# Kernel tuning notes

Hardware: AMD Instinct MI355X
Metric: run time of the kernel (lower is better)

The kernel has to match this reference:

```python
import jax, jax.numpy as jnp
import numpy as np

B, T, C = 32, 512, 32
D, H, DFF, NL = 512, 8, 2048, 3
P, STRIDE, PAD = 16, 8, 8
N = (T - P) // STRIDE + 2  # 64 patches
E = D // H


def _sinusoidal_pe(n, d):
    pos = np.arange(n, dtype=np.float32)[:, None]
    div = np.exp(np.arange(0, d, 2, dtype=np.float32) * -(np.log(10000.0) / d))
    pe = np.zeros((n, d), np.float32)
    pe[:, 0::2] = np.sin(pos * div)
    pe[:, 1::2] = np.cos(pos * div)
    return jnp.asarray(pe)


def setup_inputs() -> dict:
    key = jax.random.key(0)
    ks = jax.random.split(key, 16)
    s = 0.02
    inp = {
        'x_enc': jax.random.normal(ks[0], (B, T, C), jnp.float32),
        'W_val': jax.random.normal(ks[1], (P, D), jnp.float32) * s,
        'Wq': jax.random.normal(ks[2], (NL, D, D), jnp.float32) * s,
        'bq': jnp.zeros((NL, D), jnp.float32),
        'Wk': jax.random.normal(ks[3], (NL, D, D), jnp.float32) * s,
        'bk': jnp.zeros((NL, D), jnp.float32),
        'Wv': jax.random.normal(ks[4], (NL, D, D), jnp.float32) * s,
        'bv': jnp.zeros((NL, D), jnp.float32),
        'Wo': jax.random.normal(ks[5], (NL, D, D), jnp.float32) * s,
        'bo': jnp.zeros((NL, D), jnp.float32),
        'Wc1': jax.random.normal(ks[6], (NL, D, DFF), jnp.float32) * s,
        'bc1': jnp.zeros((NL, DFF), jnp.float32),
        'Wc2': jax.random.normal(ks[7], (NL, DFF, D), jnp.float32) * s,
        'bc2': jnp.zeros((NL, D), jnp.float32),
        'ln1_g': jnp.ones((NL, D), jnp.float32),
        'ln1_b': jnp.zeros((NL, D), jnp.float32),
        'ln2_g': jnp.ones((NL, D), jnp.float32),
        'ln2_b': jnp.zeros((NL, D), jnp.float32),
        'bn_g': jnp.ones((D,), jnp.float32),
        'bn_b': jnp.zeros((D,), jnp.float32),
        'W_head': jax.random.normal(ks[8], (D * N, T), jnp.float32) * s,
        'b_head': jnp.zeros((T,), jnp.float32),
    }
    return inp


def _ln(x, g, b, eps=1e-5):
    m = x.mean(-1, keepdims=True)
    v = ((x - m) ** 2).mean(-1, keepdims=True)
    return (x - m) / jnp.sqrt(v + eps) * g + b


def reference(x_enc, W_val, Wq, bq, Wk, bk, Wv, bv, Wo, bo, Wc1, bc1, Wc2, bc2,
              ln1_g, ln1_b, ln2_g, ln2_b, bn_g, bn_b, W_head, b_head):
    pe = _sinusoidal_pe(N, D)
    # instance normalization over time (means detached, as in torch .detach())
    means = jax.lax.stop_gradient(x_enc.mean(axis=1, keepdims=True))
    x = x_enc - means
    stdev = jnp.sqrt(x.var(axis=1, keepdims=True) + 1e-5)  # [B,1,C]
    x = x / stdev
    x = x.transpose(0, 2, 1)  # [B, C, T]
    # replication pad right by PAD, then unfold into patches [B,C,N,P]
    x = jnp.concatenate([x, jnp.broadcast_to(x[..., -1:], x.shape[:-1] + (PAD,))], axis=-1)
    idx = jnp.arange(N)[:, None] * STRIDE + jnp.arange(P)[None, :]
    xp = x[..., idx]
    tok = xp.reshape(B * C, N, P) @ W_val + pe  # [B*C, N, D]

    scale = 1.0 / np.sqrt(E).astype(np.float32)
    for i in range(NL):
        q = (tok @ Wq[i] + bq[i]).reshape(-1, N, H, E)
        k = (tok @ Wk[i] + bk[i]).reshape(-1, N, H, E)
        v = (tok @ Wv[i] + bv[i]).reshape(-1, N, H, E)
        scores = jnp.einsum('blhe,bshe->bhls', q, k)
        A = jax.nn.softmax(scale * scores, axis=-1)
        V = jnp.einsum('bhls,bshd->blhd', A, v).reshape(-1, N, D)
        tok = tok + (V @ Wo[i] + bo[i])
        y = _ln(tok, ln1_g[i], ln1_b[i])
        y = jax.nn.gelu(y @ Wc1[i] + bc1[i], approximate=False) @ Wc2[i] + bc2[i]
        tok = _ln(tok + y, ln2_g[i], ln2_b[i])

    # BatchNorm1d over d_model channels (batch statistics, biased variance)
    m = tok.mean(axis=(0, 1))
    var = tok.var(axis=(0, 1))
    tok = (tok - m) / jnp.sqrt(var + 1e-5) * bn_g + bn_b

    enc = tok.reshape(B, C, N, D).transpose(0, 1, 3, 2).reshape(B, C, D * N)
    dec = enc @ W_head + b_head          # [B, C, T]
    dec = dec.transpose(0, 2, 1)          # [B, T, C]
    dec = dec * stdev[:, 0, :][:, None, :] + means[:, 0, :][:, None, :]
    return dec
```

## Files before the change

### kernel.cpp

```cpp
#include <hip/hip_runtime.h>
#include <math.h>

namespace {
constexpr int kB = 32, kT = 512, kC = 32, kD = 512, kDFF = 2048, kNL = 3;
constexpr int kP = 16, kStride = 8, kN = 64;
constexpr int kR = kB * kC;
constexpr int kM = kR * kN;
constexpr size_t kWbElems = (size_t)1536 * 512 + 512 * 512 + 2048 * 512 + 512 * 2048;
}

typedef unsigned short u16;
typedef __attribute__((ext_vector_type(8))) short short8;
typedef __attribute__((ext_vector_type(4))) float f32x4;

__device__ __forceinline__ float b2f(u16 u) {
    return __uint_as_float(((unsigned int)u) << 16);
}
__device__ __forceinline__ u16 f2b(float f) {
    unsigned int x = __float_as_uint(f);
    return (u16)((x + 0x7fffu + ((x >> 16) & 1u)) >> 16);
}

__device__ __forceinline__ void async_copy16(const u16* g, u16* l) {
    __builtin_amdgcn_global_load_lds(
        (const __attribute__((address_space(1))) unsigned int*)g,
        (__attribute__((address_space(3))) unsigned int*)l, 16, 0, 0);
}

__global__ void fill_kernel(float* __restrict__ p, float val, int n)
{
    int i = blockIdx.x * blockDim.x + threadIdx.x;
    if (i < n) p[i] = val;
}

__global__ __launch_bounds__(256) void instnorm_stats_kernel(
    const float* __restrict__ x, float* __restrict__ means, float* __restrict__ stdev)
{
    int b = blockIdx.x;
    int c = threadIdx.x & 31;
    int g = threadIdx.x >> 5;
    float s = 0.f, sq = 0.f;
    for (int t = g; t < kT; t += 8) {
        float v = x[(size_t)(b * kT + t) * kC + c];
        s += v; sq += v * v;
    }
    __shared__ float ss[8][32], ssq[8][32];
    ss[g][c] = s; ssq[g][c] = sq;
    __syncthreads();
    if (g == 0) {
        float S = 0.f, SQ = 0.f;
        for (int i = 0; i < 8; i++) { S += ss[i][c]; SQ += ssq[i][c]; }
        float m = S / kT;
        float var = SQ / kT - m * m;
        means[b * kC + c] = m;
        stdev[b * kC + c] = sqrtf(var + 1e-5f);
    }
}

__global__ __launch_bounds__(256) void patch_embed_kernel(
    const float* __restrict__ x, const float* __restrict__ Wval,
    const float* __restrict__ means, const float* __restrict__ stdev,
    u16* __restrict__ tok)
{
    int m = blockIdx.x;
    int r = m >> 6, n = m & 63;
    int b = r >> 5, c = r & 31;
    __shared__ float patch[kP];
    if (threadIdx.x < kP) {
        int t = n * kStride + threadIdx.x;
        if (t > kT - 1) t = kT - 1;
        patch[threadIdx.x] = (x[(size_t)(b * kT + t) * kC + c] - means[r]) / stdev[r];
    }
    __syncthreads();
    for (int d = threadIdx.x; d < kD; d += 256) {
        float acc = 0.f;
        #pragma unroll
        for (int p = 0; p < kP; p++) acc += patch[p] * Wval[p * kD + d];
        int j = d >> 1;
        float freq = expf(-(float)(2 * j) * (9.210340371976184f / (float)kD));
        float ang = (float)n * freq;
        float pe = (d & 1) ? cosf(ang) : sinf(ang);
        tok[(size_t)m * kD + d] = f2b(acc + pe);
    }
}

__global__ __launch_bounds__(256) void transpose_cvt_kernel(
    const float* __restrict__ in, u16* __restrict__ outp,
    int ldi, int ldo, int zin, int zout)
{
    __shared__ float tile[64][65];
    const float* ib = in + (size_t)blockIdx.z * zin;
    u16* ob = outp + (size_t)blockIdx.z * zout;
    int k0 = blockIdx.x * 64, n0 = blockIdx.y * 64;
    int tn = threadIdx.x & 63, tk0 = threadIdx.x >> 6;
    #pragma unroll
    for (int kk = tk0; kk < 64; kk += 4)
        tile[kk][tn] = ib[(size_t)(k0 + kk) * ldi + n0 + tn];
    __syncthreads();
    int wk = threadIdx.x & 63, wn0 = threadIdx.x >> 6;
    #pragma unroll
    for (int nn = wn0; nn < 64; nn += 4)
        ob[(size_t)(n0 + nn) * ldo + k0 + wk] = f2b(tile[wk][nn]);
}

template<int EPI>
__device__ __forceinline__ void gemm_body(
    const u16* __restrict__ A, const u16* __restrict__ B,
    const float* __restrict__ bias, const float* __restrict__ auxb1,
    const float* __restrict__ auxb2,
    u16* __restrict__ C0, u16* __restrict__ C1, u16* __restrict__ C2,
    float* __restrict__ fout,
    int K, int lda, int ldb, int ldc)
{
    __shared__ alignas(16) u16 As[128 * 64];
    __shared__ alignas(16) u16 Bs[128 * 64];

    const int tid  = threadIdx.x;
    const int lane = tid & 63;
    const int wave = tid >> 6;
    const int wm   = wave >> 1;
    const int wn   = wave & 1;

    const int nwg  = gridDim.x * gridDim.y;
    const int orig = blockIdx.y * gridDim.x + blockIdx.x;
    const int qq = nwg >> 3, rr = nwg & 7;
    const int xcd = orig & 7, loc = orig >> 3;
    const int wg  = (xcd < rr) ? (xcd * (qq + 1) + loc)
                               : (rr * (qq + 1) + (xcd - rr) * qq + loc);
    const int row0 = (wg / gridDim.x) * 128;
    const int col0 = (wg % gridDim.x) * 128;
    const size_t zoff = (size_t)blockIdx.z * K;

    const int srow = tid >> 3;
    const int scol = (((tid & 7) ^ (srow & 7)) << 3);
    const u16* const Ag = A + (size_t)(row0 + srow) * lda + zoff + scol;
    const u16* const Bg = B + (size_t)(col0 + srow) * ldb + zoff + scol;
    u16* const AsW = As + (wave << 9);
    u16* const BsW = Bs + (wave << 9);

    const int fr = lane & 15;
    const int pc = (lane >> 4) ^ (lane & 7);
    const int a0 = ((wm << 6) + fr) * 64 + (pc << 3);
    const int a1 = ((wm << 6) + fr) * 64 + ((pc ^ 4) << 3);
    const int b0 = ((wn << 6) + fr) * 64 + (pc << 3);
    const int b1 = ((wn << 6) + fr) * 64 + ((pc ^ 4) << 3);

    short8 af[4], bfr[4];
    f32x4 acc[4][4];
    #pragma unroll
    for (int i = 0; i < 4; i++)
        #pragma unroll
        for (int j = 0; j < 4; j++)
            acc[i][j] = (f32x4){0.f, 0.f, 0.f, 0.f};

    for (int kb = 0; kb < K; kb += 64) {
        __syncthreads();
        #pragma unroll
        for (int c = 0; c < 4; c++) {
            async_copy16(Ag + kb + (size_t)(c * 32) * lda, AsW + c * 2048);
            async_copy16(Bg + kb + (size_t)(c * 32) * ldb, BsW + c * 2048);
        }
        __syncthreads();
        #pragma unroll
        for (int mi = 0; mi < 4; mi++) af[mi]  = *(const short8*)&As[a0 + (mi << 10)];
        #pragma unroll
        for (int ni = 0; ni < 4; ni++) bfr[ni] = *(const short8*)&Bs[b0 + (ni << 10)];
        #pragma unroll
        for (int mi = 0; mi < 4; mi++)
            #pragma unroll
            for (int ni = 0; ni < 4; ni++)
                acc[mi][ni] = __builtin_amdgcn_mfma_f32_16x16x32_bf16(
                    af[mi], bfr[ni], acc[mi][ni], 0, 0, 0);
        #pragma unroll
        for (int mi = 0; mi < 4; mi++) af[mi]  = *(const short8*)&As[a1 + (mi << 10)];
        #pragma unroll
        for (int ni = 0; ni < 4; ni++) bfr[ni] = *(const short8*)&Bs[b1 + (ni << 10)];
        #pragma unroll
        for (int mi = 0; mi < 4; mi++)
            #pragma unroll
            for (int ni = 0; ni < 4; ni++)
                acc[mi][ni] = __builtin_amdgcn_mfma_f32_16x16x32_bf16(
                    af[mi], bfr[ni], acc[mi][ni], 0, 0, 0);
    }

    const int er = (lane >> 4) << 2;
    const int ec = lane & 15;
    u16* dsel = C0;
    const float* bsel = bias;
    if (EPI == 0) {
        int sub = col0 >> 9;
        dsel = (sub == 0) ? C0 : ((sub == 1) ? C1 : C2);
        bsel = (sub == 0) ? bias : ((sub == 1) ? auxb1 : auxb2);
    }
    #pragma unroll
    for (int mi = 0; mi < 4; mi++) {
        #pragma unroll
        for (int ni = 0; ni < 4; ni++) {
            #pragma unroll
            for (int i = 0; i < 4; i++) {
                int r  = row0 + (wm << 6) + (mi << 4) + er + i;
                int cc = col0 + (wn << 6) + (ni << 4) + ec;
                float v = acc[mi][ni][i];
                if (EPI == 0) {
                    int cl = cc & 511;
                    dsel[(size_t)r * 512 + cl] = f2b(v + bsel[cl]);
                } else if (EPI == 1) {
                    size_t o = (size_t)r * ldc + cc;
                    float bb2 = bias ? bias[cc] : 0.f;
                    C0[o] = f2b(b2f(C0[o]) + v + bb2);
                } else if (EPI == 2) {
                    size_t o = (size_t)r * ldc + cc;
                    float z = v + bias[cc];
                    C0[o] = f2b(0.5f * z * (1.f + erff(z * 0.7071067811865475f)));
                } else {
                    fout[((size_t)blockIdx.z << 19) + (size_t)r * ldc + cc] = v;
                }
            }
        }
    }
}

#define GEMM_ARGS \
    const u16* __restrict__ A, const u16* __restrict__ B, \
    const float* __restrict__ bias, const float* __restrict__ auxb1, \
    const float* __restrict__ auxb2, \
    u16* __restrict__ C0, u16* __restrict__ C1, u16* __restrict__ C2, \
    float* __restrict__ fout, \
    int K, int lda, int ldb, int ldc
#define GEMM_PASS A, B, bias, auxb1, auxb2, C0, C1, C2, fout, K, lda, ldb, ldc

__global__ __launch_bounds__(256) void gemm_qkv(GEMM_ARGS)   { gemm_body<0>(GEMM_PASS); }
__global__ __launch_bounds__(256) void gemm_resid(GEMM_ARGS) { gemm_body<1>(GEMM_PASS); }
__global__ __launch_bounds__(256) void gemm_gelu(GEMM_ARGS)  { gemm_body<2>(GEMM_PASS); }
__global__ __launch_bounds__(256) void gemm_head(GEMM_ARGS)  { gemm_body<3>(GEMM_PASS); }

__global__ __launch_bounds__(256) void vtr_kernel(u16* __restrict__ v)
{
    __shared__ u16 tl[4][64 * 72];
    const int tid = threadIdx.x;
    const int wave = tid >> 6, lane = tid & 63;
    const int sr = lane >> 3, ch = lane & 7;
    const int tile = blockIdx.x * 4 + wave;
    const int series = tile >> 3, h = tile & 7;
    u16* g = v + (size_t)series * 64 * kD + h * 64;
    u16* T = tl[wave];
    short8 rd[8];
    #pragma unroll
    for (int r = 0; r < 8; r++)
        rd[r] = *(const short8*)(g + (size_t)(r * 8 + sr) * kD + ch * 8);
    #pragma unroll
    for (int r = 0; r < 8; r++)
        *(short8*)&T[(r * 8 + sr) * 72 + ch * 8] = rd[r];
    __syncthreads();
    #pragma unroll
    for (int r = 0; r < 8; r++) {
        short8 wr;
        #pragma unroll
        for (int q = 0; q < 8; q++)
            wr[q] = (short)T[(ch * 8 + q) * 72 + (r * 8 + sr)];
        *(short8*)(g + (size_t)(r * 8 + sr) * kD + ch * 8) = wr;
    }
}

__global__ __launch_bounds__(256) void attn_mfma_kernel(
    u16* __restrict__ qbuf, const u16* __restrict__ kbuf,
    const u16* __restrict__ vbuf)
{
    __shared__ u16 P[4][64 * 64];
    const int tid = threadIdx.x;
    const int wave = tid >> 6, lane = tid & 63;
    const int quad = lane >> 4, l15 = lane & 15;
    const size_t base = (size_t)blockIdx.x * 64 * kD;
    u16* Pw = P[wave];

    for (int hh = 0; hh < 2; hh++) {
        const int h = wave * 2 + hh;
        const u16* qh = qbuf + base + h * 64;
        const u16* kh = kbuf + base + h * 64;
        const u16* vh = vbuf + base + h * 64;

        short8 af[4][2], bf[4][2];
        #pragma unroll
        for (int mi = 0; mi < 4; mi++)
            #pragma unroll
            for (int kt = 0; kt < 2; kt++)
                af[mi][kt] = *(const short8*)(qh + (size_t)(mi * 16 + l15) * kD
                                              + kt * 32 + quad * 8);
        #pragma unroll
        for (int ni = 0; ni < 4; ni++)
            #pragma unroll
            for (int kt = 0; kt < 2; kt++)
                bf[ni][kt] = *(const short8*)(kh + (size_t)(ni * 16 + l15) * kD
                                              + kt * 32 + quad * 8);
        f32x4 S[4][4];
        #pragma unroll
        for (int mi = 0; mi < 4; mi++)
            #pragma unroll
            for (int ni = 0; ni < 4; ni++)
                S[mi][ni] = (f32x4){0.f, 0.f, 0.f, 0.f};
        #pragma unroll
        for (int mi = 0; mi < 4; mi++)
            #pragma unroll
            for (int ni = 0; ni < 4; ni++) {
                S[mi][ni] = __builtin_amdgcn_mfma_f32_16x16x32_bf16(
                    af[mi][0], bf[ni][0], S[mi][ni], 0, 0, 0);
                S[mi][ni] = __builtin_amdgcn_mfma_f32_16x16x32_bf16(
                    af[mi][1], bf[ni][1], S[mi][ni], 0, 0, 0);
            }

        #pragma unroll
        for (int mi = 0; mi < 4; mi++) {
            #pragma unroll
            for (int i = 0; i < 4; i++) {
                float mx = -1e30f;
                #pragma unroll
                for (int ni = 0; ni < 4; ni++) {
                    float v = S[mi][ni][i] * 0.125f;
                    S[mi][ni][i] = v;
                    mx = fmaxf(mx, v);
                }
                #pragma unroll
                for (int off = 1; off < 16; off <<= 1)
                    mx = fmaxf(mx, __shfl_xor(mx, off));
                float sum = 0.f;
                #pragma unroll
                for (int ni = 0; ni < 4; ni++) {
                    float e = expf(S[mi][ni][i] - mx);
                    S[mi][ni][i] = e;
                    sum += e;
                }
                #pragma unroll
                for (int off = 1; off < 16; off <<= 1)
                    sum += __shfl_xor(sum, off);
                float inv = 1.f / sum;
                #pragma unroll
                for (int ni = 0; ni < 4; ni++)
                    Pw[(mi * 16 + quad * 4 + i) * 64 + ni * 16 + l15] =
                        f2b(S[mi][ni][i] * inv);
            }
        }
        __syncthreads();

        short8 bv[4][2];
        #pragma unroll
        for (int ni = 0; ni < 4; ni++)
            #pragma unroll
            for (int kt = 0; kt < 2; kt++)
                bv[ni][kt] = *(const short8*)(vh + (size_t)(ni * 16 + l15) * kD
                                              + kt * 32 + quad * 8);
        short8 pa[4][2];
        #pragma unroll
        for (int mi = 0; mi < 4; mi++)
            #pragma unroll
            for (int kt = 0; kt < 2; kt++)
                pa[mi][kt] = *(const short8*)&Pw[(mi * 16 + l15) * 64
                                                 + kt * 32 + quad * 8];
        f32x4 O[4][4];
        #pragma unroll
        for (int mi = 0; mi < 4; mi++)
            #pragma unroll
            for (int ni = 0; ni < 4; ni++)
                O[mi][ni] = (f32x4){0.f, 0.f, 0.f, 0.f};
        #pragma unroll
        for (int mi = 0; mi < 4; mi++)
            #pragma unroll
            for (int ni = 0; ni < 4; ni++) {
                O[mi][ni] = __builtin_amdgcn_mfma_f32_16x16x32_bf16(
                    pa[mi][0], bv[ni][0], O[mi][ni], 0, 0, 0);
                O[mi][ni] = __builtin_amdgcn_mfma_f32_16x16x32_bf16(
                    pa[mi][1], bv[ni][1], O[mi][ni], 0, 0, 0);
            }
        u16* qo = qbuf + base + h * 64;
        #pragma unroll
        for (int mi = 0; mi < 4; mi++)
            #pragma unroll
            for (int ni = 0; ni < 4; ni++)
                #pragma unroll
                for (int i = 0; i < 4; i++)
                    qo[(size_t)(mi * 16 + quad * 4 + i) * kD + ni * 16 + l15] =
                        f2b(O[mi][ni][i]);
        __syncthreads();
    }
}

__global__ __launch_bounds__(256) void ln_kernel(
    const u16* __restrict__ x, const float* __restrict__ g,
    const float* __restrict__ bb, u16* __restrict__ y)
{
    size_t row = (size_t)blockIdx.x * 4 + (threadIdx.x >> 6);
    int lane = threadIdx.x & 63;
    float v[8];
    float s = 0.f;
    #pragma unroll
    for (int i = 0; i < 8; i++) {
        v[i] = b2f(x[row * kD + lane + i * 64]);
        s += v[i];
    }
    #pragma unroll
    for (int off = 32; off; off >>= 1) s += __shfl_xor(s, off);
    float mean = s * (1.f / kD);
    float sq = 0.f;
    #pragma unroll
    for (int i = 0; i < 8; i++) { float d = v[i] - mean; sq += d * d; }
    #pragma unroll
    for (int off = 32; off; off >>= 1) sq += __shfl_xor(sq, off);
    float inv = 1.f / sqrtf(sq * (1.f / kD) + 1e-5f);
    #pragma unroll
    for (int i = 0; i < 8; i++) {
        int d = lane + i * 64;
        y[row * kD + d] = f2b((v[i] - mean) * inv * g[d] + bb[d]);
    }
}

__global__ void zero_kernel(float* __restrict__ p, int n)
{
    int i = blockIdx.x * blockDim.x + threadIdx.x;
    if (i < n) p[i] = 0.f;
}

__global__ __launch_bounds__(512) void bn_stats_kernel(
    const u16* __restrict__ tok, float* __restrict__ sums, float* __restrict__ sumsq)
{
    int d = threadIdx.x;
    float s = 0.f, sq = 0.f;
    int row0 = blockIdx.x * 256;
    for (int row = row0; row < row0 + 256; row++) {
        float v = b2f(tok[(size_t)row * kD + d]);
        s += v; sq += v * v;
    }
    atomicAdd(&sums[d], s);
    atomicAdd(&sumsq[d], sq);
}

__global__ __launch_bounds__(512) void bn_final_kernel(
    const float* __restrict__ sums, const float* __restrict__ sumsq,
    const float* __restrict__ g, const float* __restrict__ bb,
    float* __restrict__ scale, float* __restrict__ shift)
{
    int d = threadIdx.x;
    float mean = sums[d] / (float)kM;
    float var = sumsq[d] / (float)kM - mean * mean;
    float sc = g[d] / sqrtf(var + 1e-5f);
    scale[d] = sc;
    shift[d] = bb[d] - mean * sc;
}

__global__ __launch_bounds__(256) void bn_apply_kernel(
    u16* __restrict__ tok, const float* __restrict__ scale,
    const float* __restrict__ shift)
{
    size_t i = (size_t)blockIdx.x * 256 + threadIdx.x;
    int d = (int)(i & 511);
    tok[i] = f2b(b2f(tok[i]) * scale[d] + shift[d]);
}

__global__ __launch_bounds__(256) void head_reduce_kernel(
    const float* __restrict__ part, const float* __restrict__ b_head,
    const float* __restrict__ stdev, const float* __restrict__ means,
    float* __restrict__ out)
{
    int j = blockIdx.x * 256 + threadIdx.x;
    int r = j >> 9, t = j & 511;
    float s = 0.f;
    #pragma unroll
    for (int z = 0; z < 16; z++) s += part[((size_t)z << 19) + j];
    int b = r >> 5, c = r & 31;
    out[(((size_t)b * kT + t) << 5) + c] = (s + b_head[t]) * stdev[r] + means[r];
}

extern "C" void kernel_launch(void* const* d_in, const int* in_sizes, int n_in,
                              void* d_out, int out_size, void* d_ws, size_t ws_size,
                              hipStream_t stream)
{
    const float* x_enc  = (const float*)d_in[0];
    const float* W_val  = (const float*)d_in[1];
    const float* Wq     = (const float*)d_in[2];
    const float* bq     = (const float*)d_in[3];
    const float* Wk     = (const float*)d_in[4];
    const float* bk     = (const float*)d_in[5];
    const float* Wv     = (const float*)d_in[6];
    const float* bv     = (const float*)d_in[7];
    const float* Wo     = (const float*)d_in[8];
    const float* bo     = (const float*)d_in[9];
    const float* Wc1    = (const float*)d_in[10];
    const float* bc1    = (const float*)d_in[11];
    const float* Wc2    = (const float*)d_in[12];
    const float* bc2    = (const float*)d_in[13];
    const float* ln1_g  = (const float*)d_in[14];
    const float* ln1_b  = (const float*)d_in[15];
    const float* ln2_g  = (const float*)d_in[16];
    const float* ln2_b  = (const float*)d_in[17];
    const float* bn_g   = (const float*)d_in[18];
    const float* bn_b   = (const float*)d_in[19];
    const float* W_head = (const float*)d_in[20];
    const float* b_head = (const float*)d_in[21];
    float* out = (float*)d_out;

    const size_t tailBytes = (2 * kR + 4 * kD) * sizeof(float);
    const size_t headWb = (size_t)512 * 32768;
    int CH = 0; size_t unit = 0, region = 0;
    const int cands[4] = {1024, 512, 256, 128};
    for (int ci = 0; ci < 4; ci++) {
        size_t u = (size_t)cands[ci] * 64 * kD;
        size_t reg = 3 * u + kWbElems;
        if (reg < headWb) reg = headWb;
        size_t need = ((size_t)kM * kD + reg) * 2 + tailBytes;
        if (need <= ws_size) { CH = cands[ci]; unit = u; region = reg; break; }
    }
    if (CH == 0) {
        hipLaunchKernelGGL(fill_kernel, dim3((out_size + 255) / 256), dim3(256), 0,
                           stream, out, 1.0e6f, out_size);
        return;
    }
    const int nch = kR / CH;
    const int chRows = CH * 64;

    u16* tokb = (u16*)d_ws;
    u16* s0  = tokb + (size_t)kM * kD;
    u16* s1  = s0 + unit;
    u16* s2  = s1 + unit;
    u16* wbL = s2 + unit;
    u16* wbH = s0;
    u16* wQKV = wbL;
    u16* wO   = wQKV + (size_t)1536 * 512;
    u16* wC1  = wO + (size_t)512 * 512;
    u16* wC2  = wC1 + (size_t)2048 * 512;
    float* tail = (float*)(s0 + region);
    float* means    = tail;
    float* stdevp   = means + kR;
    float* bn_sums  = stdevp + kR;
    float* bn_sumsq = bn_sums + kD;
    float* bn_scale = bn_sumsq + kD;
    float* bn_shift = bn_scale + kD;

    hipLaunchKernelGGL(instnorm_stats_kernel, dim3(kB), dim3(256), 0, stream,
                       x_enc, means, stdevp);
    hipLaunchKernelGGL(patch_embed_kernel, dim3(kM), dim3(256), 0, stream,
                       x_enc, W_val, means, stdevp, tokb);

    const dim3 blk(256);
    const dim3 tr8(8, 8, 1);
    const int mt = chRows / 128;

    for (int i = 0; i < kNL; i++) {
        const float* Wq_i = Wq + (size_t)i * kD * kD;
        const float* Wk_i = Wk + (size_t)i * kD * kD;
        const float* Wv_i = Wv + (size_t)i * kD * kD;
        const float* Wo_i = Wo + (size_t)i * kD * kD;
        const float* Wc1_i = Wc1 + (size_t)i * kD * kDFF;
        const float* Wc2_i = Wc2 + (size_t)i * kDFF * kD;
        const float* bq_i = bq + i * kD, *bk_i = bk + i * kD, *bv_i = bv + i * kD;

        hipLaunchKernelGGL(transpose_cvt_kernel, tr8, blk, 0, stream,
                           Wq_i, wQKV, kD, kD, 0, 0);
        hipLaunchKernelGGL(transpose_cvt_kernel, tr8, blk, 0, stream,
                           Wk_i, wQKV + (size_t)512 * 512, kD, kD, 0, 0);
        hipLaunchKernelGGL(transpose_cvt_kernel, tr8, blk, 0, stream,
                           Wv_i, wQKV + (size_t)1024 * 512, kD, kD, 0, 0);
        hipLaunchKernelGGL(transpose_cvt_kernel, tr8, blk, 0, stream,
                           Wo_i, wO, kD, kD, 0, 0);
        hipLaunchKernelGGL(transpose_cvt_kernel, dim3(8, 32, 1), blk, 0, stream,
                           Wc1_i, wC1, kDFF, kD, 0, 0);
        hipLaunchKernelGGL(transpose_cvt_kernel, dim3(32, 8, 1), blk, 0, stream,
                           Wc2_i, wC2, kD, kDFF, 0, 0);

        for (int ch = 0; ch < nch; ch++) {
            u16* tokc = tokb + (size_t)ch * chRows * kD;
            hipLaunchKernelGGL(gemm_qkv, dim3(12, mt, 1), blk, 0, stream,
                               tokc, wQKV, bq_i, bk_i, bv_i, s0, s1, s2,
                               nullptr, kD, kD, kD, kD);
            hipLaunchKernelGGL(vtr_kernel, dim3(CH * 2), blk, 0, stream, s2);
            hipLaunchKernelGGL(attn_mfma_kernel, dim3(CH), blk, 0, stream,
                               s0, s1, s2);
            hipLaunchKernelGGL(gemm_resid, dim3(4, mt, 1), blk, 0, stream,
                               s0, wO, bo + i * kD, nullptr, nullptr,
                               tokc, nullptr, nullptr, nullptr,
                               kD, kD, kD, kD);
            hipLaunchKernelGGL(ln_kernel, dim3(chRows / 4), blk, 0, stream,
                               tokc, ln1_g + i * kD, ln1_b + i * kD, s0);
            for (int half = 0; half < 2; half++) {
                const u16* wc1h = wC1 + (size_t)half * 1024 * 512;
                const u16* wc2h = wC2 + (size_t)half * 1024;
                const float* bc1h = bc1 + (size_t)i * kDFF + half * 1024;
                hipLaunchKernelGGL(gemm_gelu, dim3(8, mt, 1), blk, 0, stream,
                                   s0, wc1h, bc1h, nullptr, nullptr,
                                   s1, nullptr, nullptr, nullptr,
                                   kD, kD, kD, 1024);
                hipLaunchKernelGGL(gemm_resid, dim3(4, mt, 1), blk, 0, stream,
                                   s1, wc2h, (half == 0) ? (bc2 + i * kD) : nullptr,
                                   nullptr, nullptr, tokc, nullptr, nullptr,
                                   nullptr, 1024, 1024, kDFF, kD);
            }
            hipLaunchKernelGGL(ln_kernel, dim3(chRows / 4), blk, 0, stream,
                               tokc, ln2_g + i * kD, ln2_b + i * kD, tokc);
        }
    }

    hipLaunchKernelGGL(zero_kernel, dim3(1), dim3(1024), 0, stream, bn_sums, 2 * kD);
    hipLaunchKernelGGL(bn_stats_kernel, dim3(kM / 256), dim3(512), 0, stream,
                       tokb, bn_sums, bn_sumsq);
    hipLaunchKernelGGL(bn_final_kernel, dim3(1), dim3(512), 0, stream,
                       bn_sums, bn_sumsq, bn_g, bn_b, bn_scale, bn_shift);
    hipLaunchKernelGGL(bn_apply_kernel, dim3((int)((size_t)kM * kD / 256)), blk, 0,
                       stream, tokb, bn_scale, bn_shift);

    hipLaunchKernelGGL(transpose_cvt_kernel, dim3(8, 8, 64), blk, 0, stream,
                       W_head, wbH, 64 * 512, 32768, 512, 512);
    hipLaunchKernelGGL(gemm_head, dim3(4, 8, 16), blk, 0, stream,
                       tokb, wbH, nullptr, nullptr, nullptr,
                       nullptr, nullptr, nullptr, (float*)s1,
                       2048, 32768, 32768, kT);
    hipLaunchKernelGGL(head_reduce_kernel, dim3(kR * kT / 256), blk, 0, stream,
                       (const float*)s1, b_head, stdevp, means, out);
}
```

Before: 3.237 ms.

## Fold BatchNorm affine into head weights and precompute positional encoding table

Removes the full-size BatchNorm apply pass over the token buffer. The per-channel scale is folded into the head weight while it is transposed and converted, and the shift is folded into a per-output bias computed from W_head. The sinusoidal positional encoding is now computed once into a small table instead of per token, and the four QKV/O weight transposes are merged into one launch. The trade-off is an extra reduction kernel over W_head, plus slightly different rounding because the bf16 head weights now carry the scale.

```diff
diff --git a/kernel.cpp b/kernel.cpp
--- a/kernel.cpp
+++ b/kernel.cpp
@@ -57,10 +57,20 @@
     }
 }
 
+__global__ __launch_bounds__(256) void pe_kernel(float* __restrict__ pe)
+{
+    int i = blockIdx.x * 256 + threadIdx.x;
+    int n = i >> 9, d = i & 511;
+    int j = d >> 1;
+    float freq = expf(-(float)(2 * j) * (9.210340371976184f / (float)kD));
+    float ang = (float)n * freq;
+    pe[i] = (d & 1) ? cosf(ang) : sinf(ang);
+}
+
 __global__ __launch_bounds__(256) void patch_embed_kernel(
     const float* __restrict__ x, const float* __restrict__ Wval,
     const float* __restrict__ means, const float* __restrict__ stdev,
-    u16* __restrict__ tok)
+    const float* __restrict__ pe, u16* __restrict__ tok)
 {
     int m = blockIdx.x;
     int r = m >> 6, n = m & 63;
@@ -72,20 +82,18 @@
         patch[threadIdx.x] = (x[(size_t)(b * kT + t) * kC + c] - means[r]) / stdev[r];
     }
     __syncthreads();
+    const float* pen = pe + (size_t)n * kD;
     for (int d = threadIdx.x; d < kD; d += 256) {
         float acc = 0.f;
         #pragma unroll
         for (int p = 0; p < kP; p++) acc += patch[p] * Wval[p * kD + d];
-        int j = d >> 1;
-        float freq = expf(-(float)(2 * j) * (9.210340371976184f / (float)kD));
-        float ang = (float)n * freq;
-        float pe = (d & 1) ? cosf(ang) : sinf(ang);
-        tok[(size_t)m * kD + d] = f2b(acc + pe);
+        tok[(size_t)m * kD + d] = f2b(acc + pen[d]);
     }
 }
 
 __global__ __launch_bounds__(256) void transpose_cvt_kernel(
     const float* __restrict__ in, u16* __restrict__ outp,
+    const float* __restrict__ scale,
     int ldi, int ldo, int zin, int zout)
 {
     __shared__ float tile[64][65];
@@ -94,13 +102,36 @@
     int k0 = blockIdx.x * 64, n0 = blockIdx.y * 64;
     int tn = threadIdx.x & 63, tk0 = threadIdx.x >> 6;
     #pragma unroll
-    for (int kk = tk0; kk < 64; kk += 4)
-        tile[kk][tn] = ib[(size_t)(k0 + kk) * ldi + n0 + tn];
+    for (int kk = tk0; kk < 64; kk += 4) {
+        float sc = scale ? scale[k0 + kk] : 1.f;
+        tile[kk][tn] = ib[(size_t)(k0 + kk) * ldi + n0 + tn] * sc;
+    }
     __syncthreads();
     int wk = threadIdx.x & 63, wn0 = threadIdx.x >> 6;
     #pragma unroll
     for (int nn = wn0; nn < 64; nn += 4)
         ob[(size_t)(n0 + nn) * ldo + k0 + wk] = f2b(tile[wk][nn]);
+}
+
+__global__ __launch_bounds__(256) void transpose_cvt4_kernel(
+    const float* __restrict__ in0, const float* __restrict__ in1,
+    const float* __restrict__ in2, const float* __restrict__ in3,
+    u16* __restrict__ outQKV, u16* __restrict__ outO)
+{
+    __shared__ float tile[64][65];
+    int z = blockIdx.z;
+    const float* ib = (z == 0) ? in0 : (z == 1) ? in1 : (z == 2) ? in2 : in3;
+    u16* ob = (z < 3) ? outQKV + (size_t)z * 512 * 512 : outO;
+    int k0 = blockIdx.x * 64, n0 = blockIdx.y * 64;
+    int tn = threadIdx.x & 63, tk0 = threadIdx.x >> 6;
+    #pragma unroll
+    for (int kk = tk0; kk < 64; kk += 4)
+        tile[kk][tn] = ib[(size_t)(k0 + kk) * 512 + n0 + tn];
+    __syncthreads();
+    int wk = threadIdx.x & 63, wn0 = threadIdx.x >> 6;
+    #pragma unroll
+    for (int nn = wn0; nn < 64; nn += 4)
+        ob[(size_t)(n0 + nn) * 512 + k0 + wk] = f2b(tile[wk][nn]);
 }
 
 template<int EPI>
@@ -445,17 +476,21 @@
     shift[d] = bb[d] - mean * sc;
 }
 
-__global__ __launch_bounds__(256) void bn_apply_kernel(
-    u16* __restrict__ tok, const float* __restrict__ scale,
-    const float* __restrict__ shift)
-{
-    size_t i = (size_t)blockIdx.x * 256 + threadIdx.x;
-    int d = (int)(i & 511);
-    tok[i] = f2b(b2f(tok[i]) * scale[d] + shift[d]);
+__global__ __launch_bounds__(512) void head_shift_kernel(
+    const float* __restrict__ W_head, const float* __restrict__ shift,
+    float* __restrict__ shiftW)
+{
+    int t = threadIdx.x;
+    int r0 = blockIdx.x * 512;
+    float s = 0.f;
+    for (int r = r0; r < r0 + 512; r++)
+        s += shift[r >> 6] * W_head[(size_t)r * 512 + t];
+    atomicAdd(&shiftW[t], s);
 }
 
 __global__ __launch_bounds__(256) void head_reduce_kernel(
     const float* __restrict__ part, const float* __restrict__ b_head,
+    const float* __restrict__ shiftW,
     const float* __restrict__ stdev, const float* __restrict__ means,
     float* __restrict__ out)
 {
@@ -465,7 +500,8 @@
     #pragma unroll
     for (int z = 0; z < 16; z++) s += part[((size_t)z << 19) + j];
     int b = r >> 5, c = r & 31;
-    out[(((size_t)b * kT + t) << 5) + c] = (s + b_head[t]) * stdev[r] + means[r];
+    out[(((size_t)b * kT + t) << 5) + c] =
+        (s + shiftW[t] + b_head[t]) * stdev[r] + means[r];
 }
 
 extern "C" void kernel_launch(void* const* d_in, const int* in_sizes, int n_in,
@@ -496,7 +532,7 @@
     const float* b_head = (const float*)d_in[21];
     float* out = (float*)d_out;
 
-    const size_t tailBytes = (2 * kR + 4 * kD) * sizeof(float);
+    const size_t tailBytes = (2 * kR + 5 * kD + 64 * kD) * sizeof(float);
     const size_t headWb = (size_t)512 * 32768;
     int CH = 0; size_t unit = 0, region = 0;
     const int cands[4] = {1024, 512, 256, 128};
@@ -530,16 +566,18 @@
     float* stdevp   = means + kR;
     float* bn_sums  = stdevp + kR;
     float* bn_sumsq = bn_sums + kD;
-    float* bn_scale = bn_sumsq + kD;
+    float* shiftW   = bn_sumsq + kD;
+    float* bn_scale = shiftW + kD;
     float* bn_shift = bn_scale + kD;
-
+    float* peT      = bn_shift + kD;
+
+    hipLaunchKernelGGL(pe_kernel, dim3(128), dim3(256), 0, stream, peT);
     hipLaunchKernelGGL(instnorm_stats_kernel, dim3(kB), dim3(256), 0, stream,
                        x_enc, means, stdevp);
     hipLaunchKernelGGL(patch_embed_kernel, dim3(kM), dim3(256), 0, stream,
-                       x_enc, W_val, means, stdevp, tokb);
+                       x_enc, W_val, means, stdevp, peT, tokb);
 
     const dim3 blk(256);
-    const dim3 tr8(8, 8, 1);
     const int mt = chRows / 128;
 
     for (int i = 0; i < kNL; i++) {
@@ -551,18 +589,12 @@
         const float* Wc2_i = Wc2 + (size_t)i * kDFF * kD;
         const float* bq_i = bq + i * kD, *bk_i = bk + i * kD, *bv_i = bv + i * kD;
 
-        hipLaunchKernelGGL(transpose_cvt_kernel, tr8, blk, 0, stream,
-                           Wq_i, wQKV, kD, kD, 0, 0);
-        hipLaunchKernelGGL(transpose_cvt_kernel, tr8, blk, 0, stream,
-                           Wk_i, wQKV + (size_t)512 * 512, kD, kD, 0, 0);
-        hipLaunchKernelGGL(transpose_cvt_kernel, tr8, blk, 0, stream,
-                           Wv_i, wQKV + (size_t)1024 * 512, kD, kD, 0, 0);
-        hipLaunchKernelGGL(transpose_cvt_kernel, tr8, blk, 0, stream,
-                           Wo_i, wO, kD, kD, 0, 0);
+        hipLaunchKernelGGL(transpose_cvt4_kernel, dim3(8, 8, 4), blk, 0, stream,
+                           Wq_i, Wk_i, Wv_i, Wo_i, wQKV, wO);
         hipLaunchKernelGGL(transpose_cvt_kernel, dim3(8, 32, 1), blk, 0, stream,
-                           Wc1_i, wC1, kDFF, kD, 0, 0);
+                           Wc1_i, wC1, nullptr, kDFF, kD, 0, 0);
         hipLaunchKernelGGL(transpose_cvt_kernel, dim3(32, 8, 1), blk, 0, stream,
-                           Wc2_i, wC2, kD, kDFF, 0, 0);
+                           Wc2_i, wC2, nullptr, kD, kDFF, 0, 0);
 
         for (int ch = 0; ch < nch; ch++) {
             u16* tokc = tokb + (size_t)ch * chRows * kD;
@@ -596,20 +628,20 @@
         }
     }
 
-    hipLaunchKernelGGL(zero_kernel, dim3(1), dim3(1024), 0, stream, bn_sums, 2 * kD);
+    hipLaunchKernelGGL(zero_kernel, dim3(6), dim3(256), 0, stream, bn_sums, 3 * kD);
     hipLaunchKernelGGL(bn_stats_kernel, dim3(kM / 256), dim3(512), 0, stream,
                        tokb, bn_sums, bn_sumsq);
     hipLaunchKernelGGL(bn_final_kernel, dim3(1), dim3(512), 0, stream,
                        bn_sums, bn_sumsq, bn_g, bn_b, bn_scale, bn_shift);
-    hipLaunchKernelGGL(bn_apply_kernel, dim3((int)((size_t)kM * kD / 256)), blk, 0,
-                       stream, tokb, bn_scale, bn_shift);
+    hipLaunchKernelGGL(head_shift_kernel, dim3(64), dim3(512), 0, stream,
+                       W_head, bn_shift, shiftW);
 
     hipLaunchKernelGGL(transpose_cvt_kernel, dim3(8, 8, 64), blk, 0, stream,
-                       W_head, wbH, 64 * 512, 32768, 512, 512);
+                       W_head, wbH, bn_scale, 64 * 512, 32768, 512, 512);
     hipLaunchKernelGGL(gemm_head, dim3(4, 8, 16), blk, 0, stream,
                        tokb, wbH, nullptr, nullptr, nullptr,
                        nullptr, nullptr, nullptr, (float*)s1,
                        2048, 32768, 32768, kT);
     hipLaunchKernelGGL(head_reduce_kernel, dim3(kR * kT / 256), blk, 0, stream,
-                       (const float*)s1, b_head, stdevp, means, out);
-}
+                       (const float*)s1, b_head, shiftW, stdevp, means, out);
+}
```

Measured after the change: 3.214 ms. About the same (-0.7%).
